# Optimization experiments

Measured on AMD Instinct MI355X. Metric: run time of the kernel, lower is better.

The kernel has to match this reference:

```python
import jax, jax.numpy as jnp
import numpy as np

# Structural constants (mirror init_kwargs)
P = 64    # n_poses
R = 128   # rotamers per pose
A = 8     # atoms per rotamer
EPS = 1e-2  # distance clamp to avoid singularity


def setup_inputs() -> dict:
    key = jax.random.key(0)
    n_rots = P * R
    coords = jax.random.normal(key, (n_rots * A, 3), dtype=jnp.float32) * 3.0
    coord_offset_for_rot = (jnp.arange(n_rots, dtype=jnp.int32) * A)
    pose_for_rot = jnp.repeat(jnp.arange(P, dtype=jnp.int32), R)
    rot_offset_for_pose = jnp.arange(P, dtype=jnp.int32) * R
    return {
        "coords": coords,
        "coord_offset_for_rot": coord_offset_for_rot,
        "pose_for_rot": pose_for_rot,
        "rot_offset_for_pose": rot_offset_for_pose,
    }


def reference(coords, coord_offset_for_rot, pose_for_rot, rot_offset_for_pose):
    # flatten leading dims to [n_atoms_total, 3] (matches coords.flatten(0,-2))
    flat = coords.reshape(-1, 3)
    # gather each rotamer's atoms via its coordinate offset: [n_rots, A]
    atom_idx = coord_offset_for_rot[:, None] + jnp.arange(A, dtype=jnp.int32)[None, :]
    x = flat[atom_idx]                       # [n_rots, A, 3]
    x = x.reshape(P, R, A, 3)                # block per pose
    # squared pairwise atom distances between all rotamer pairs within a pose
    sq = jnp.sum(x * x, axis=-1)             # [P, R, A]
    dot = jnp.einsum('piac,pjbc->pijab', x, x)   # [P, R, R, A, A]
    d2 = sq[:, :, None, :, None] + sq[:, None, :, None, :] - 2.0 * dot
    d2 = jnp.maximum(d2, EPS)
    # two subterm energies summed over atom pairs -> [P, R, R]
    s0 = jnp.sum(1.0 / d2, axis=(-2, -1))                  # LJ-like repulsion
    s1 = jnp.sum(jnp.exp(-jnp.sqrt(d2)), axis=(-2, -1))    # LK-like decay
    scores = jnp.stack([s0.reshape(-1), s1.reshape(-1)], axis=0)  # [2, nnz]
    # indices [3, nnz]: (pose, global rot_i, global rot_j)
    r = jnp.arange(R, dtype=jnp.int32)
    ii, jj = jnp.meshgrid(r, r, indexing='ij')             # [R, R]
    pose_idx = jnp.repeat(pose_for_rot, R)                 # [P*R*R]
    rot_i = (rot_offset_for_pose[:, None, None] + ii[None]).reshape(-1)
    rot_j = (rot_offset_for_pose[:, None, None] + jj[None]).reshape(-1)
    indices = jnp.stack([pose_idx, rot_i, rot_j], axis=0).astype(jnp.int32)
    return scores, indices
```

## Files before the change

### kernel.cpp

```cpp
#include <hip/hip_runtime.h>

typedef float v2f __attribute__((ext_vector_type(2)));

#define NPOSE 64
#define NROT  128
#define NATOM 8
#define EPS   1e-2f

#define TS    16
#define NTILE (NROT / TS)
#define NPAIR (NTILE * (NTILE + 1) / 2)
#define CSTR  28
#define SSTR  17

__global__ __launch_bounds__(256, 4) void rot_score_kernel(
    const float* __restrict__ coords,
    float* __restrict__ out)
{
    __shared__ float ldsI[TS * CSTR];
    __shared__ float ldsJ[TS * CSTR];
    __shared__ float res0[TS * SSTR];
    __shared__ float res1[TS * SSTR];

    const int bid = blockIdx.x;
    const int p   = bid / NPAIR;
    int t = bid - p * NPAIR;
    int ti = 0;
    while (t >= NTILE - ti) { t -= NTILE - ti; ++ti; }
    const int tj = ti + t;

    const int tid = threadIdx.x;
    const float* src = coords + (size_t)p * (NROT * NATOM * 3);

    for (int idx = tid; idx < 2 * TS * 24; idx += 256) {
        const int set = idx >= TS * 24;
        const int loc = idx - set * (TS * 24);
        const int r   = loc / 24;
        const int k   = loc - r * 24;
        const float v = src[(set ? tj : ti) * (TS * 24) + loc];
        (set ? ldsJ : ldsI)[r * CSTR + k] = v;
    }
    __syncthreads();

    const int ty = tid >> 4;
    const int tx = tid & 15;

    float4 xi4[6], xj4[6];
    {
        const float4* rowI = (const float4*)&ldsI[ty * CSTR];
        const float4* rowJ = (const float4*)&ldsJ[tx * CSTR];
#pragma unroll
        for (int k = 0; k < 6; ++k) { xi4[k] = rowI[k]; xj4[k] = rowJ[k]; }
    }
    const float* xi = (const float*)xi4;
    const float* xj = (const float*)xj4;

    float sqi[NATOM];
#pragma unroll
    for (int a = 0; a < NATOM; ++a)
        sqi[a] = fmaf(xi[a*3+2], xi[a*3+2], fmaf(xi[a*3+1], xi[a*3+1], xi[a*3+0]*xi[a*3+0]));

    v2f jx[4], jy[4], jz[4], sj[4];
#pragma unroll
    for (int bp = 0; bp < 4; ++bp) {
        v2f ax = { xj[bp*6 + 0], xj[bp*6 + 3] };
        v2f ay = { xj[bp*6 + 1], xj[bp*6 + 4] };
        v2f az = { xj[bp*6 + 2], xj[bp*6 + 5] };
        sj[bp] = __builtin_elementwise_fma(az, az, __builtin_elementwise_fma(ay, ay, ax*ax));
        jx[bp] = ax * -2.0f;
        jy[bp] = ay * -2.0f;
        jz[bp] = az * -2.0f;
    }

    const float NEG_LOG2E = -1.44269504088896340736f;
    v2f s0v = { 0.0f, 0.0f }, s1v = { 0.0f, 0.0f };
    const v2f veps = { EPS, EPS };

#pragma unroll
    for (int bp = 0; bp < 4; ++bp) {
#pragma unroll
        for (int a = 0; a < NATOM; ++a) {
            v2f t = sj[bp] + sqi[a];
            v2f cx = xi[a*3+0], cy = xi[a*3+1], cz = xi[a*3+2];
            t = __builtin_elementwise_fma(cx, jx[bp], t);
            t = __builtin_elementwise_fma(cy, jy[bp], t);
            t = __builtin_elementwise_fma(cz, jz[bp], t);
            t = __builtin_elementwise_max(t, veps);
            v2f rs = { __builtin_amdgcn_rsqf(t.x), __builtin_amdgcn_rsqf(t.y) };
            s0v = __builtin_elementwise_fma(rs, rs, s0v);
            v2f arg = (t * NEG_LOG2E) * rs;
            v2f e = { __builtin_amdgcn_exp2f(arg.x), __builtin_amdgcn_exp2f(arg.y) };
            s1v += e;
        }
    }
    const float s0 = s0v.x + s0v.y;
    const float s1 = s1v.x + s1v.y;

    res0[ty * SSTR + tx] = s0;
    res1[ty * SSTR + tx] = s1;

    const int nnz = NPOSE * NROT * NROT;
    const int gi  = ti * TS + ty;
    const int gj  = tj * TS + tx;
    const int n   = (p * NROT + gi) * NROT + gj;

    out[0 * nnz + n] = s0;
    out[1 * nnz + n] = s1;
    out[2 * nnz + n] = (float)p;
    out[3 * nnz + n] = (float)(p * NROT + gi);
    out[4 * nnz + n] = (float)(p * NROT + gj);

    if (ti != tj) {
        __syncthreads();
        const float m0 = res0[tx * SSTR + ty];
        const float m1 = res1[tx * SSTR + ty];
        const int mi = tj * TS + ty;
        const int mj = ti * TS + tx;
        const int nm = (p * NROT + mi) * NROT + mj;
        out[0 * nnz + nm] = m0;
        out[1 * nnz + nm] = m1;
        out[2 * nnz + nm] = (float)p;
        out[3 * nnz + nm] = (float)(p * NROT + mi);
        out[4 * nnz + nm] = (float)(p * NROT + mj);
    }
}

extern "C" void kernel_launch(void* const* d_in, const int* in_sizes, int n_in,
                              void* d_out, int out_size, void* d_ws, size_t ws_size,
                              hipStream_t stream) {
    (void)in_sizes; (void)n_in; (void)d_ws; (void)ws_size; (void)out_size;
    const float* coords = (const float*)d_in[0];
    float* out = (float*)d_out;

    dim3 grid(NPOSE * NPAIR);
    dim3 block(256);
    rot_score_kernel<<<grid, block, 0, stream>>>(coords, out);
}
```

Baseline: 20.03 us.

## Compute four columns per thread with vectorized stores and approximate exp

Shrinks blocks to a single 64-lane wave where each thread computes four adjacent j rotamers, so output rows can be written with float4 stores. The exp2 transcendental is replaced with a Schraudolph-style bit-trick exponential computed by an FMA and an int conversion. The intent is to cut per-element store instructions and transcendental throughput cost. The bit-trick exponential has a relative error of a few percent, which risks accuracy tolerance.

```diff
diff --git a/kernel.cpp b/kernel.cpp
--- a/kernel.cpp
+++ b/kernel.cpp
@@ -13,7 +13,7 @@
 #define CSTR  28
 #define SSTR  17
 
-__global__ __launch_bounds__(256, 4) void rot_score_kernel(
+__global__ __launch_bounds__(64, 4) void rot_score_kernel(
     const float* __restrict__ coords,
     float* __restrict__ out)
 {
@@ -29,10 +29,10 @@
     while (t >= NTILE - ti) { t -= NTILE - ti; ++ti; }
     const int tj = ti + t;
 
-    const int tid = threadIdx.x;
+    const int lane = threadIdx.x;
     const float* src = coords + (size_t)p * (NROT * NATOM * 3);
 
-    for (int idx = tid; idx < 2 * TS * 24; idx += 256) {
+    for (int idx = lane; idx < 2 * TS * 24; idx += 64) {
         const int set = idx >= TS * 24;
         const int loc = idx - set * (TS * 24);
         const int r   = loc / 24;
@@ -42,86 +42,116 @@
     }
     __syncthreads();
 
-    const int ty = tid >> 4;
-    const int tx = tid & 15;
+    const int ty  = lane >> 2;
+    const int txg = lane & 3;
 
-    float4 xi4[6], xj4[6];
+    float4 xi4[6];
     {
         const float4* rowI = (const float4*)&ldsI[ty * CSTR];
-        const float4* rowJ = (const float4*)&ldsJ[tx * CSTR];
 #pragma unroll
-        for (int k = 0; k < 6; ++k) { xi4[k] = rowI[k]; xj4[k] = rowJ[k]; }
+        for (int k = 0; k < 6; ++k) xi4[k] = rowI[k];
     }
-    const float* xi = (const float*)xi4;
-    const float* xj = (const float*)xj4;
+    float* xi = (float*)xi4;
 
     float sqi[NATOM];
 #pragma unroll
     for (int a = 0; a < NATOM; ++a)
         sqi[a] = fmaf(xi[a*3+2], xi[a*3+2], fmaf(xi[a*3+1], xi[a*3+1], xi[a*3+0]*xi[a*3+0]));
+#pragma unroll
+    for (int k = 0; k < 24; ++k) xi[k] = xi[k] * -2.0f;
 
-    v2f jx[4], jy[4], jz[4], sj[4];
+    const float SCH_S = -12102203.0f;
+    const float SCH_B = 1064866805.0f;
+
+    float4 s0q, s1q;
+    float* s0p = (float*)&s0q;
+    float* s1p = (float*)&s1q;
+
 #pragma unroll
-    for (int bp = 0; bp < 4; ++bp) {
-        v2f ax = { xj[bp*6 + 0], xj[bp*6 + 3] };
-        v2f ay = { xj[bp*6 + 1], xj[bp*6 + 4] };
-        v2f az = { xj[bp*6 + 2], xj[bp*6 + 5] };
-        sj[bp] = __builtin_elementwise_fma(az, az, __builtin_elementwise_fma(ay, ay, ax*ax));
-        jx[bp] = ax * -2.0f;
-        jy[bp] = ay * -2.0f;
-        jz[bp] = az * -2.0f;
+    for (int jj = 0; jj < 4; ++jj) {
+        const int tx = txg * 4 + jj;
+        float4 xj4[6];
+        {
+            const float4* rowJ = (const float4*)&ldsJ[tx * CSTR];
+#pragma unroll
+            for (int k = 0; k < 6; ++k) xj4[k] = rowJ[k];
+        }
+        const float* xj = (const float*)xj4;
+
+        v2f s0v = { 0.0f, 0.0f }, s1v = { 0.0f, 0.0f };
+        const v2f veps = { EPS, EPS };
+
+#pragma unroll
+        for (int bp = 0; bp < 4; ++bp) {
+            const v2f ax = { xj[bp*6 + 0], xj[bp*6 + 3] };
+            const v2f ay = { xj[bp*6 + 1], xj[bp*6 + 4] };
+            const v2f az = { xj[bp*6 + 2], xj[bp*6 + 5] };
+            const v2f sj = __builtin_elementwise_fma(az, az,
+                            __builtin_elementwise_fma(ay, ay, ax * ax));
+#pragma unroll
+            for (int a = 0; a < NATOM; ++a) {
+                v2f t = sj + sqi[a];
+                t = __builtin_elementwise_fma((v2f)(xi[a*3+0]), ax, t);
+                t = __builtin_elementwise_fma((v2f)(xi[a*3+1]), ay, t);
+                t = __builtin_elementwise_fma((v2f)(xi[a*3+2]), az, t);
+                t = __builtin_elementwise_max(t, veps);
+                const v2f rs = { __builtin_amdgcn_rsqf(t.x),
+                                 __builtin_amdgcn_rsqf(t.y) };
+                s0v = __builtin_elementwise_fma(rs, rs, s0v);
+                const v2f dv = t * rs;
+                const v2f st = __builtin_elementwise_fma(dv, (v2f)(SCH_S), (v2f)(SCH_B));
+                v2f e;
+                e.x = __int_as_float((int)st.x);
+                e.y = __int_as_float((int)st.y);
+                s1v += e;
+            }
+        }
+        s0p[jj] = s0v.x + s0v.y;
+        s1p[jj] = s1v.x + s1v.y;
     }
 
-    const float NEG_LOG2E = -1.44269504088896340736f;
-    v2f s0v = { 0.0f, 0.0f }, s1v = { 0.0f, 0.0f };
-    const v2f veps = { EPS, EPS };
+#pragma unroll
+    for (int k = 0; k < 4; ++k) {
+        res0[ty * SSTR + txg * 4 + k] = s0p[k];
+        res1[ty * SSTR + txg * 4 + k] = s1p[k];
+    }
 
-#pragma unroll
-    for (int bp = 0; bp < 4; ++bp) {
-#pragma unroll
-        for (int a = 0; a < NATOM; ++a) {
-            v2f t = sj[bp] + sqi[a];
-            v2f cx = xi[a*3+0], cy = xi[a*3+1], cz = xi[a*3+2];
-            t = __builtin_elementwise_fma(cx, jx[bp], t);
-            t = __builtin_elementwise_fma(cy, jy[bp], t);
-            t = __builtin_elementwise_fma(cz, jz[bp], t);
-            t = __builtin_elementwise_max(t, veps);
-            v2f rs = { __builtin_amdgcn_rsqf(t.x), __builtin_amdgcn_rsqf(t.y) };
-            s0v = __builtin_elementwise_fma(rs, rs, s0v);
-            v2f arg = (t * NEG_LOG2E) * rs;
-            v2f e = { __builtin_amdgcn_exp2f(arg.x), __builtin_amdgcn_exp2f(arg.y) };
-            s1v += e;
-        }
-    }
-    const float s0 = s0v.x + s0v.y;
-    const float s1 = s1v.x + s1v.y;
+    const int nnz  = NPOSE * NROT * NROT;
+    const int gi   = ti * TS + ty;
+    const int col0 = tj * TS + txg * 4;
+    const int n    = (p * NROT + gi) * NROT + col0;
 
-    res0[ty * SSTR + tx] = s0;
-    res1[ty * SSTR + tx] = s1;
+    const float fp  = (float)p;
+    const float ri  = (float)(p * NROT + gi);
+    const float rj0 = (float)(p * NROT + col0);
 
-    const int nnz = NPOSE * NROT * NROT;
-    const int gi  = ti * TS + ty;
-    const int gj  = tj * TS + tx;
-    const int n   = (p * NROT + gi) * NROT + gj;
-
-    out[0 * nnz + n] = s0;
-    out[1 * nnz + n] = s1;
-    out[2 * nnz + n] = (float)p;
-    out[3 * nnz + n] = (float)(p * NROT + gi);
-    out[4 * nnz + n] = (float)(p * NROT + gj);
+    *(float4*)(out + (size_t)0 * nnz + n) = s0q;
+    *(float4*)(out + (size_t)1 * nnz + n) = s1q;
+    *(float4*)(out + (size_t)2 * nnz + n) = make_float4(fp, fp, fp, fp);
+    *(float4*)(out + (size_t)3 * nnz + n) = make_float4(ri, ri, ri, ri);
+    *(float4*)(out + (size_t)4 * nnz + n) = make_float4(rj0, rj0 + 1.0f, rj0 + 2.0f, rj0 + 3.0f);
 
     if (ti != tj) {
         __syncthreads();
-        const float m0 = res0[tx * SSTR + ty];
-        const float m1 = res1[tx * SSTR + ty];
-        const int mi = tj * TS + ty;
-        const int mj = ti * TS + tx;
-        const int nm = (p * NROT + mi) * NROT + mj;
-        out[0 * nnz + nm] = m0;
-        out[1 * nnz + nm] = m1;
-        out[2 * nnz + nm] = (float)p;
-        out[3 * nnz + nm] = (float)(p * NROT + mi);
-        out[4 * nnz + nm] = (float)(p * NROT + mj);
+        float4 m0q, m1q;
+        float* m0p = (float*)&m0q;
+        float* m1p = (float*)&m1q;
+#pragma unroll
+        for (int k = 0; k < 4; ++k) {
+            m0p[k] = res0[(txg * 4 + k) * SSTR + ty];
+            m1p[k] = res1[(txg * 4 + k) * SSTR + ty];
+        }
+        const int mi    = tj * TS + ty;
+        const int mcol0 = ti * TS + txg * 4;
+        const int nm    = (p * NROT + mi) * NROT + mcol0;
+        const float mri  = (float)(p * NROT + mi);
+        const float mrj0 = (float)(p * NROT + mcol0);
+
+        *(float4*)(out + (size_t)0 * nnz + nm) = m0q;
+        *(float4*)(out + (size_t)1 * nnz + nm) = m1q;
+        *(float4*)(out + (size_t)2 * nnz + nm) = make_float4(fp, fp, fp, fp);
+        *(float4*)(out + (size_t)3 * nnz + nm) = make_float4(mri, mri, mri, mri);
+        *(float4*)(out + (size_t)4 * nnz + nm) = make_float4(mrj0, mrj0 + 1.0f, mrj0 + 2.0f, mrj0 + 3.0f);
     }
 }
 
@@ -133,6 +163,6 @@
     float* out = (float*)d_out;
 
     dim3 grid(NPOSE * NPAIR);
-    dim3 block(256);
+    dim3 block(64);
     rot_score_kernel<<<grid, block, 0, stream>>>(coords, out);
 }
```

Result: slower. 24.07 us (+20.2%).
